# Kernel optimization log

Hardware: AMD Instinct MI355X
Metric: run time of the kernel (lower is better)

The kernel has to match this reference:

```python
import jax, jax.numpy as jnp
import numpy as np

N_CLASSES = 1000
FEAT_DIM = 256
N = 65536


def setup_inputs() -> dict:
    key = jax.random.key(0)
    k1, k2, k3 = jax.random.split(key, 3)
    gt = jax.random.randint(k1, (N, N_CLASSES), 0, 2, dtype=jnp.int32)
    features = jax.random.normal(k2, (N, FEAT_DIM), dtype=jnp.float32)
    centers = jax.random.normal(k3, (N_CLASSES, FEAT_DIM), dtype=jnp.float32)
    return {"gt": gt, "features": features, "centers": centers}


def reference(gt, features, centers):
    # loss = (1/N) * sum_c sum_{i : gt[i,c] > 0} ||features[i] - centers[c]||^2
    # Vectorized via ||f||^2 + ||c||^2 - 2 f.c  (replaces the per-class python loop)
    mask = (gt > 0).astype(features.dtype)                      # [N, C]
    f_sq = jnp.sum(features * features, axis=1)                 # [N]
    c_sq = jnp.sum(centers * centers, axis=1)                   # [C]
    cross = features @ centers.T                                # [N, C]
    dist = f_sq[:, None] + c_sq[None, :] - 2.0 * cross          # [N, C]
    num_instances = features.shape[0]
    return jnp.sum(mask * dist) / num_instances
```

## Files before the change

### kernel.cpp

```cpp
#include <hip/hip_runtime.h>
#include <hip/hip_bf16.h>
#include <stdint.h>

#define N_ROWS 65536
#define N_CLS  1000
#define KPAD   1024
#define FEAT   256
#define MT     64
#define BK     64
#define NIT    (KPAD/BK)
#define LDA    72
#define LDB    72

typedef short bf16x8 __attribute__((ext_vector_type(8)));
typedef float f32x4  __attribute__((ext_vector_type(4)));

__device__ __forceinline__ ushort f32_to_bf16_rne(float f) {
    union { float f; uint32_t u; } x; x.f = f;
    uint32_t u = x.u + 0x7FFFu + ((x.u >> 16) & 1u);
    return (ushort)(u >> 16);
}

__global__ __launch_bounds__(256) void prep_kernel(const float* __restrict__ centers,
                                                   ushort* __restrict__ centersT,
                                                   float* __restrict__ csq,
                                                   float* __restrict__ out) {
    const int c = blockIdx.x;
    const int n = threadIdx.x;
    float v = 0.f;
    if (c < N_CLS) v = centers[(size_t)c * FEAT + n];
    centersT[(size_t)n * KPAD + c] = f32_to_bf16_rne(v);
    float sq = v * v;
    #pragma unroll
    for (int off = 32; off > 0; off >>= 1) sq += __shfl_down(sq, off);
    __shared__ float red[4];
    if ((threadIdx.x & 63) == 0) red[threadIdx.x >> 6] = sq;
    __syncthreads();
    if (threadIdx.x == 0) {
        csq[c] = red[0] + red[1] + red[2] + red[3];
        if (c == 0) out[0] = 0.f;
    }
}

__global__ __launch_bounds__(256) void main_kernel(const int* __restrict__ gt,
                                                   const float* __restrict__ features,
                                                   const ushort* __restrict__ centersT,
                                                   const float* __restrict__ csq,
                                                   float* __restrict__ out) {
    __shared__ ushort As[MT * LDA];
    __shared__ ushort Bs[FEAT * LDB];
    __shared__ float  rcS[256];
    __shared__ float  t2S[256];
    __shared__ float  rowcnt[MT];
    __shared__ float  t2row[MT];
    __shared__ float  blockred[4];

    const int tid  = threadIdx.x;
    const int m0   = blockIdx.x * MT;
    const int r    = tid >> 2;
    const int kc   = tid & 3;
    const int lane = tid & 63;
    const int w    = tid >> 6;
    const int ml   = lane & 15;
    const int quad = lane >> 4;

    f32x4 acc[4][4];
    #pragma unroll
    for (int i = 0; i < 4; i++)
        #pragma unroll
        for (int j = 0; j < 4; j++)
            #pragma unroll
            for (int k = 0; k < 4; k++) acc[i][j][k] = 0.f;

    float rc = 0.f, t2 = 0.f;
    const int* gtrow = gt + (size_t)(m0 + r) * N_CLS;

    for (int it = 0; it < NIT; ++it) {
        const int k0 = it * BK;
        __syncthreads();

        const int kb = k0 + kc * 16;
        int v[16];
        if (kb + 16 <= N_CLS) {
            const int4* p = (const int4*)(gtrow + kb);
            int4 a0 = p[0], a1 = p[1], a2 = p[2], a3 = p[3];
            v[0]=a0.x; v[1]=a0.y; v[2]=a0.z; v[3]=a0.w;
            v[4]=a1.x; v[5]=a1.y; v[6]=a1.z; v[7]=a1.w;
            v[8]=a2.x; v[9]=a2.y; v[10]=a2.z; v[11]=a2.w;
            v[12]=a3.x; v[13]=a3.y; v[14]=a3.z; v[15]=a3.w;
        } else {
            #pragma unroll
            for (int j = 0; j < 16; j++) {
                int k = kb + j;
                v[j] = (k < N_CLS) ? gtrow[k] : 0;
            }
        }
        float cs[16];
        {
            const float4* cp = (const float4*)(csq + kb);
            float4 q0 = cp[0], q1 = cp[1], q2 = cp[2], q3 = cp[3];
            cs[0]=q0.x; cs[1]=q0.y; cs[2]=q0.z; cs[3]=q0.w;
            cs[4]=q1.x; cs[5]=q1.y; cs[6]=q1.z; cs[7]=q1.w;
            cs[8]=q2.x; cs[9]=q2.y; cs[10]=q2.z; cs[11]=q2.w;
            cs[12]=q3.x; cs[13]=q3.y; cs[14]=q3.z; cs[15]=q3.w;
        }
        uint32_t u[8];
        #pragma unroll
        for (int j = 0; j < 8; j++) {
            uint32_t lo = (v[2*j]   > 0) ? 0x3F80u : 0u;
            uint32_t hi = (v[2*j+1] > 0) ? 0x3F80u : 0u;
            u[j] = lo | (hi << 16);
        }
        #pragma unroll
        for (int j = 0; j < 16; j++) {
            bool m = v[j] > 0;
            rc += m ? 1.f : 0.f;
            t2 += m ? cs[j] : 0.f;
        }
        {
            uint4* dst = (uint4*)&As[r * LDA + kc * 16];
            dst[0] = make_uint4(u[0], u[1], u[2], u[3]);
            dst[1] = make_uint4(u[4], u[5], u[6], u[7]);
        }

        #pragma unroll
        for (int j = 0; j < 8; j++) {
            int g = j * 256 + tid;
            int n = g >> 3;
            int kcb = g & 7;
            *(uint4*)&Bs[n * LDB + kcb * 8] =
                *(const uint4*)&centersT[(size_t)n * KPAD + k0 + kcb * 8];
        }

        __syncthreads();

        #pragma unroll
        for (int ks = 0; ks < 2; ++ks) {
            const int kk = ks * 32 + quad * 8;
            bf16x8 af[4], bfr[4];
            #pragma unroll
            for (int mt = 0; mt < 4; mt++)
                af[mt] = *(const bf16x8*)&As[(mt * 16 + ml) * LDA + kk];
            #pragma unroll
            for (int nt = 0; nt < 4; nt++)
                bfr[nt] = *(const bf16x8*)&Bs[(w * 64 + nt * 16 + ml) * LDB + kk];
            #pragma unroll
            for (int mt = 0; mt < 4; mt++)
                #pragma unroll
                for (int nt = 0; nt < 4; nt++)
                    acc[mt][nt] = __builtin_amdgcn_mfma_f32_16x16x32_bf16(
                        af[mt], bfr[nt], acc[mt][nt], 0, 0, 0);
        }
    }

    rcS[tid] = rc;
    t2S[tid] = t2;
    __syncthreads();
    if (tid < MT) {
        rowcnt[tid] = rcS[tid*4] + rcS[tid*4+1] + rcS[tid*4+2] + rcS[tid*4+3];
        t2row[tid]  = t2S[tid*4] + t2S[tid*4+1] + t2S[tid*4+2] + t2S[tid*4+3];
    }
    __syncthreads();

    float part = 0.f;
    #pragma unroll
    for (int mt = 0; mt < 4; mt++) {
        #pragma unroll
        for (int nt = 0; nt < 4; nt++) {
            const int n = w * 64 + nt * 16 + ml;
            #pragma unroll
            for (int reg = 0; reg < 4; reg++) {
                const int ri = mt * 16 + quad * 4 + reg;
                const float f = features[(size_t)(m0 + ri) * FEAT + n];
                const float T = acc[mt][nt][reg];
                part += f * (rowcnt[ri] * f - 2.f * T) + t2row[ri] * (1.f / 256.f);
            }
        }
    }
    #pragma unroll
    for (int off = 32; off > 0; off >>= 1) part += __shfl_down(part, off);
    if (lane == 0) blockred[w] = part;
    __syncthreads();
    if (tid == 0)
        atomicAdd(out, (blockred[0] + blockred[1] + blockred[2] + blockred[3]) *
                           (1.f / (float)N_ROWS));
}

extern "C" void kernel_launch(void* const* d_in, const int* in_sizes, int n_in,
                              void* d_out, int out_size, void* d_ws, size_t ws_size,
                              hipStream_t stream) {
    const int*   gt       = (const int*)d_in[0];
    const float* features = (const float*)d_in[1];
    const float* centers  = (const float*)d_in[2];
    float*       out      = (float*)d_out;

    ushort* centersT = (ushort*)d_ws;
    float*  csq      = (float*)((char*)d_ws + (size_t)FEAT * KPAD * 2);

    prep_kernel<<<KPAD, 256, 0, stream>>>(centers, centersT, csq, out);
    main_kernel<<<N_ROWS / MT, 256, 0, stream>>>(gt, features, centersT, csq, out);
}
```

Measured before the change: 411.9 us.

## Switch to fp16 MFMA with XOR-swizzled LDS and packed mask arithmetic

Replaces bf16 with fp16 for the centers and mask operands and uses fp16 MFMA. Padded LDS tiles become XOR-swizzled uint4 layouts, which shrinks LDS use, and launch bounds now request 4 blocks per CU. Mask conversion uses packed integer multiply, with row counts held in packed 16-bit lanes. The ||c||^2 term is accumulated with fdot2 against fp16 center norms. This cuts VALU work and LDS footprint, but relies on gt values being exactly 0/1 and adds fp16 rounding on the centers and their norms.

Result: slower. 434.3 us (+5.4%).

```diff
diff --git a/kernel.cpp b/kernel.cpp
--- a/kernel.cpp
+++ b/kernel.cpp
@@ -1,5 +1,4 @@
 #include <hip/hip_runtime.h>
-#include <hip/hip_bf16.h>
 #include <stdint.h>
 
 #define N_ROWS 65536
@@ -9,27 +8,25 @@
 #define MT     64
 #define BK     64
 #define NIT    (KPAD/BK)
-#define LDA    72
-#define LDB    72
 
-typedef short bf16x8 __attribute__((ext_vector_type(8)));
-typedef float f32x4  __attribute__((ext_vector_type(4)));
+typedef _Float16 f16x8 __attribute__((ext_vector_type(8)));
+typedef _Float16 f16x2 __attribute__((ext_vector_type(2)));
+typedef float    f32x4 __attribute__((ext_vector_type(4)));
 
-__device__ __forceinline__ ushort f32_to_bf16_rne(float f) {
-    union { float f; uint32_t u; } x; x.f = f;
-    uint32_t u = x.u + 0x7FFFu + ((x.u >> 16) & 1u);
-    return (ushort)(u >> 16);
+__device__ __forceinline__ f16x2 as_f16x2(uint32_t u) {
+    union { uint32_t u; f16x2 h; } c; c.u = u; return c.h;
 }
 
 __global__ __launch_bounds__(256) void prep_kernel(const float* __restrict__ centers,
                                                    ushort* __restrict__ centersT,
-                                                   float* __restrict__ csq,
+                                                   ushort* __restrict__ csqh,
                                                    float* __restrict__ out) {
     const int c = blockIdx.x;
     const int n = threadIdx.x;
     float v = 0.f;
     if (c < N_CLS) v = centers[(size_t)c * FEAT + n];
-    centersT[(size_t)n * KPAD + c] = f32_to_bf16_rne(v);
+    union { _Float16 h; ushort s; } cv; cv.h = (_Float16)v;
+    centersT[(size_t)n * KPAD + c] = cv.s;
     float sq = v * v;
     #pragma unroll
     for (int off = 32; off > 0; off >>= 1) sq += __shfl_down(sq, off);
@@ -37,32 +34,30 @@
     if ((threadIdx.x & 63) == 0) red[threadIdx.x >> 6] = sq;
     __syncthreads();
     if (threadIdx.x == 0) {
-        csq[c] = red[0] + red[1] + red[2] + red[3];
+        union { _Float16 h; ushort s; } cs;
+        cs.h = (_Float16)(red[0] + red[1] + red[2] + red[3]);
+        csqh[c] = cs.s;
         if (c == 0) out[0] = 0.f;
     }
 }
 
-__global__ __launch_bounds__(256) void main_kernel(const int* __restrict__ gt,
-                                                   const float* __restrict__ features,
-                                                   const ushort* __restrict__ centersT,
-                                                   const float* __restrict__ csq,
-                                                   float* __restrict__ out) {
-    __shared__ ushort As[MT * LDA];
-    __shared__ ushort Bs[FEAT * LDB];
-    __shared__ float  rcS[256];
-    __shared__ float  t2S[256];
-    __shared__ float  rowcnt[MT];
-    __shared__ float  t2row[MT];
-    __shared__ float  blockred[4];
+__global__ __launch_bounds__(256, 4) void main_kernel(const int* __restrict__ gt,
+                                                      const float* __restrict__ features,
+                                                      const ushort* __restrict__ centersT,
+                                                      const ushort* __restrict__ csqh,
+                                                      float* __restrict__ out) {
+    __shared__ uint4 As4[MT * 8];
+    __shared__ uint4 Bs4[FEAT * 8];
 
     const int tid  = threadIdx.x;
     const int m0   = blockIdx.x * MT;
     const int r    = tid >> 2;
-    const int kc   = tid & 3;
+    const int kc2  = tid & 3;
     const int lane = tid & 63;
     const int w    = tid >> 6;
     const int ml   = lane & 15;
     const int quad = lane >> 4;
+    const int mls  = ml & 7;
 
     f32x4 acc[4][4];
     #pragma unroll
@@ -72,14 +67,16 @@
             #pragma unroll
             for (int k = 0; k < 4; k++) acc[i][j][k] = 0.f;
 
-    float rc = 0.f, t2 = 0.f;
-    const int* gtrow = gt + (size_t)(m0 + r) * N_CLS;
+    uint32_t rcp = 0;
+    float    t2  = 0.f;
+    const int*   gtrow = gt + (size_t)(m0 + r) * N_CLS;
+    const uint4* ctv   = (const uint4*)centersT;
 
     for (int it = 0; it < NIT; ++it) {
         const int k0 = it * BK;
+        const int kb = k0 + kc2 * 16;
         __syncthreads();
 
-        const int kb = k0 + kc * 16;
         int v[16];
         if (kb + 16 <= N_CLS) {
             const int4* p = (const int4*)(gtrow + kb);
@@ -95,74 +92,65 @@
                 v[j] = (k < N_CLS) ? gtrow[k] : 0;
             }
         }
-        float cs[16];
-        {
-            const float4* cp = (const float4*)(csq + kb);
-            float4 q0 = cp[0], q1 = cp[1], q2 = cp[2], q3 = cp[3];
-            cs[0]=q0.x; cs[1]=q0.y; cs[2]=q0.z; cs[3]=q0.w;
-            cs[4]=q1.x; cs[5]=q1.y; cs[6]=q1.z; cs[7]=q1.w;
-            cs[8]=q2.x; cs[9]=q2.y; cs[10]=q2.z; cs[11]=q2.w;
-            cs[12]=q3.x; cs[13]=q3.y; cs[14]=q3.z; cs[15]=q3.w;
-        }
+        uint4 cq0 = *(const uint4*)(csqh + kb);
+        uint4 cq1 = *(const uint4*)(csqh + kb + 8);
+        uint32_t cp[8] = {cq0.x, cq0.y, cq0.z, cq0.w, cq1.x, cq1.y, cq1.z, cq1.w};
+
         uint32_t u[8];
         #pragma unroll
         for (int j = 0; j < 8; j++) {
-            uint32_t lo = (v[2*j]   > 0) ? 0x3F80u : 0u;
-            uint32_t hi = (v[2*j+1] > 0) ? 0x3F80u : 0u;
-            u[j] = lo | (hi << 16);
+            uint32_t t = (uint32_t)v[2*j] + ((uint32_t)v[2*j+1] << 16);
+            rcp += t;
+            u[j] = t * 0x3C00u;
+            t2 = __builtin_amdgcn_fdot2(as_f16x2(u[j]), as_f16x2(cp[j]), t2, false);
         }
-        #pragma unroll
-        for (int j = 0; j < 16; j++) {
-            bool m = v[j] > 0;
-            rc += m ? 1.f : 0.f;
-            t2 += m ? cs[j] : 0.f;
-        }
+
         {
-            uint4* dst = (uint4*)&As[r * LDA + kc * 16];
-            dst[0] = make_uint4(u[0], u[1], u[2], u[3]);
-            dst[1] = make_uint4(u[4], u[5], u[6], u[7]);
+            uint4* dst = &As4[r * 8];
+            dst[(2*kc2)     ^ (r & 7)] = make_uint4(u[0], u[1], u[2], u[3]);
+            dst[(2*kc2 + 1) ^ (r & 7)] = make_uint4(u[4], u[5], u[6], u[7]);
         }
 
         #pragma unroll
         for (int j = 0; j < 8; j++) {
-            int g = j * 256 + tid;
-            int n = g >> 3;
-            int kcb = g & 7;
-            *(uint4*)&Bs[n * LDB + kcb * 8] =
-                *(const uint4*)&centersT[(size_t)n * KPAD + k0 + kcb * 8];
+            int g  = j * 256 + tid;
+            int n  = g >> 3;
+            int kl = g & 7;
+            Bs4[n * 8 + (kl ^ (n & 7))] = ctv[n * 128 + (k0 >> 3) + kl];
         }
 
         __syncthreads();
 
         #pragma unroll
         for (int ks = 0; ks < 2; ++ks) {
-            const int kk = ks * 32 + quad * 8;
-            bf16x8 af[4], bfr[4];
+            const int lc = ks * 4 + quad;
+            f16x8 af[4], bfr[4];
             #pragma unroll
             for (int mt = 0; mt < 4; mt++)
-                af[mt] = *(const bf16x8*)&As[(mt * 16 + ml) * LDA + kk];
+                af[mt] = ((const f16x8*)As4)[(mt * 16 + ml) * 8 + (lc ^ mls)];
             #pragma unroll
-            for (int nt = 0; nt < 4; nt++)
-                bfr[nt] = *(const bf16x8*)&Bs[(w * 64 + nt * 16 + ml) * LDB + kk];
+            for (int nt = 0; nt < 4; nt++) {
+                const int col = w * 64 + nt * 16 + ml;
+                bfr[nt] = ((const f16x8*)Bs4)[col * 8 + (lc ^ mls)];
+            }
             #pragma unroll
             for (int mt = 0; mt < 4; mt++)
                 #pragma unroll
                 for (int nt = 0; nt < 4; nt++)
-                    acc[mt][nt] = __builtin_amdgcn_mfma_f32_16x16x32_bf16(
+                    acc[mt][nt] = __builtin_amdgcn_mfma_f32_16x16x32_f16(
                         af[mt], bfr[nt], acc[mt][nt], 0, 0, 0);
         }
     }
 
-    rcS[tid] = rc;
-    t2S[tid] = t2;
     __syncthreads();
-    if (tid < MT) {
-        rowcnt[tid] = rcS[tid*4] + rcS[tid*4+1] + rcS[tid*4+2] + rcS[tid*4+3];
-        t2row[tid]  = t2S[tid*4] + t2S[tid*4+1] + t2S[tid*4+2] + t2S[tid*4+3];
-    }
+    float* S = (float*)As4;
+    S[tid] = (float)((rcp & 0xFFFFu) + (rcp >> 16));
+    __syncthreads();
+    if (tid < MT)
+        S[256 + tid] = S[tid*4] + S[tid*4+1] + S[tid*4+2] + S[tid*4+3];
     __syncthreads();
 
-    float part = 0.f;
+    float part = t2;
     #pragma unroll
     for (int mt = 0; mt < 4; mt++) {
         #pragma unroll
@@ -173,17 +161,16 @@
                 const int ri = mt * 16 + quad * 4 + reg;
                 const float f = features[(size_t)(m0 + ri) * FEAT + n];
                 const float T = acc[mt][nt][reg];
-                part += f * (rowcnt[ri] * f - 2.f * T) + t2row[ri] * (1.f / 256.f);
+                part += f * (S[256 + ri] * f - 2.f * T);
             }
         }
     }
     #pragma unroll
     for (int off = 32; off > 0; off >>= 1) part += __shfl_down(part, off);
-    if (lane == 0) blockred[w] = part;
+    if (lane == 0) S[320 + w] = part;
     __syncthreads();
     if (tid == 0)
-        atomicAdd(out, (blockred[0] + blockred[1] + blockred[2] + blockred[3]) *
-                           (1.f / (float)N_ROWS));
+        atomicAdd(out, (S[320] + S[321] + S[322] + S[323]) * (1.f / (float)N_ROWS));
 }
 
 extern "C" void kernel_launch(void* const* d_in, const int* in_sizes, int n_in,
@@ -195,8 +182,8 @@
     float*       out      = (float*)d_out;
 
     ushort* centersT = (ushort*)d_ws;
-    float*  csq      = (float*)((char*)d_ws + (size_t)FEAT * KPAD * 2);
+    ushort* csqh     = (ushort*)((char*)d_ws + (size_t)FEAT * KPAD * 2);
 
-    prep_kernel<<<KPAD, 256, 0, stream>>>(centers, centersT, csq, out);
-    main_kernel<<<N_ROWS / MT, 256, 0, stream>>>(gt, features, centersT, csq, out);
+    prep_kernel<<<KPAD, 256, 0, stream>>>(centers, centersT, csqh, out);
+    main_kernel<<<N_ROWS / MT, 256, 0, stream>>>(gt, features, centersT, csqh, out);
 }
```
